# Kernel tuning notes

Hardware: AMD Instinct MI355X
Metric: run time of the kernel (lower is better)

The kernel has to match this reference:

```python
import math
import jax, jax.numpy as jnp
import numpy as np

N_GAUSS = 1_000_000
EPS = 1e-8


def setup_inputs() -> dict:
    key = jax.random.key(0)
    k1, k2, k3 = jax.random.split(key, 3)
    init_extent = 50.0
    means = (jax.random.uniform(k1, (N_GAUSS, 3), dtype=jnp.float32) - 0.5) * 2.0 * init_extent
    log_scales = jnp.full((N_GAUSS, 3), math.log(0.05), dtype=jnp.float32)
    quats = jax.random.normal(k2, (N_GAUSS, 4), dtype=jnp.float32)
    sh_coeffs = jax.random.normal(k3, (N_GAUSS, 16, 3), dtype=jnp.float32) * 0.01
    opa_logit = math.log(0.1 / 0.9)  # inverse_sigmoid(init_opacity=0.1)
    opacity_camera = jnp.full((N_GAUSS, 1), opa_logit, dtype=jnp.float32)
    opacity_lidar = jnp.full((N_GAUSS, 1), opa_logit, dtype=jnp.float32)
    camera_to_world = jnp.eye(4, dtype=jnp.float32)
    lidar_to_world = jnp.eye(4, dtype=jnp.float32)
    intrinsics = jnp.array([[1000.0, 0.0, 800.0], [0.0, 1000.0, 450.0], [0.0, 0.0, 1.0]], dtype=jnp.float32)
    return dict(means=means, log_scales=log_scales, quats=quats, sh_coeffs=sh_coeffs,
                opacity_camera=opacity_camera, opacity_lidar=opacity_lidar,
                camera_to_world=camera_to_world, intrinsics=intrinsics,
                lidar_to_world=lidar_to_world,
                rgb_width=1600, rgb_height=900, lidar_width=1024, lidar_height=128,
                fov_min_deg=-25, fov_max_deg=3, near_plane=1, far_plane=100)


def _bilinear_scatter(u, v, w, vals, H, W, wrap_u):
    """Scatter vals [N,C] with weights w [N] at continuous pixel coords (u,v)
    using bilinear splatting. Returns [H, W, C+1] (weighted vals, weight sum)."""
    u0 = jnp.floor(u)
    v0 = jnp.floor(v)
    fu = u - u0
    fv = v - v0
    u0i = u0.astype(jnp.int32)
    v0i = v0.astype(jnp.int32)
    acc = jnp.zeros((H * W, vals.shape[-1] + 1), dtype=vals.dtype)
    corners = ((0, 0, (1.0 - fu) * (1.0 - fv)), (1, 0, fu * (1.0 - fv)),
               (0, 1, (1.0 - fu) * fv), (1, 1, fu * fv))
    for du, dv, cw in corners:
        ui = u0i + du
        vi = v0i + dv
        if wrap_u:
            ui = jnp.mod(ui, W)
            ok_u = jnp.ones_like(ui, dtype=bool)
        else:
            ok_u = (ui >= 0) & (ui < W)
        ok = ok_u & (vi >= 0) & (vi < H)
        ww = w * cw * ok.astype(w.dtype)
        idx = jnp.clip(vi, 0, H - 1) * W + jnp.clip(ui, 0, W - 1)
        payload = jnp.concatenate([vals * ww[:, None], ww[:, None]], axis=-1)
        acc = acc.at[idx].add(payload)
    return acc.reshape(H, W, -1)


def reference(means, log_scales, quats, sh_coeffs, opacity_camera, opacity_lidar,
              camera_to_world, intrinsics, lidar_to_world,
              rgb_width, rgb_height, lidar_width, lidar_height,
              fov_min_deg, fov_max_deg, near_plane, far_plane):
    H, W = int(rgb_height), int(rgb_width)
    HL, WL = int(lidar_height), int(lidar_width)
    near = float(near_plane)
    far = float(far_plane)

    # ---- camera (point-splat proxy of gsplat rasterization) ----
    w2c = jnp.linalg.inv(camera_to_world)
    pts_c = means @ w2c[:3, :3].T + w2c[:3, 3]  # [N,3] camera frame
    x, y, z = pts_c[:, 0], pts_c[:, 1], pts_c[:, 2]
    valid_c = (z > near) & (z < far)
    zs = jnp.where(valid_c, z, 1.0)
    u = intrinsics[0, 0] * x / zs + intrinsics[0, 2]
    v = intrinsics[1, 1] * y / zs + intrinsics[1, 2]
    opa_c = jax.nn.sigmoid(jnp.clip(opacity_camera[:, 0], -20.0, 20.0))
    colors = jax.nn.sigmoid(sh_coeffs[:, 0, :])  # DC band, as in render_rgb
    wc = opa_c * valid_c.astype(opa_c.dtype)
    vals_c = jnp.concatenate([colors, z[:, None]], axis=-1)  # [N,4] (rgb, depth)
    acc = _bilinear_scatter(u, v, wc, vals_c, H, W, wrap_u=False)
    wsum = acc[..., 4]
    alpha = jnp.clip(wsum, 0.0, 1.0)
    rgb = acc[..., :3] / (wsum[..., None] + EPS) * alpha[..., None]  # black background
    depth = acc[..., 3] / (wsum + EPS)

    # ---- LiDAR (custom spherical bilinear range-image splat, mean aggregation) ----
    w2l = jnp.linalg.inv(lidar_to_world)
    pts_l = means @ w2l[:3, :3].T + w2l[:3, 3]
    r = jnp.linalg.norm(pts_l, axis=-1)
    az = jnp.arctan2(pts_l[:, 1], pts_l[:, 0])
    el = jnp.arcsin(pts_l[:, 2] / jnp.maximum(r, 1e-6))
    fmin = math.radians(float(fov_min_deg))
    fmax = math.radians(float(fov_max_deg))
    uL = (az / (2.0 * jnp.pi) + 0.5) * WL          # azimuth wraps around
    vL = (fmax - el) / (fmax - fmin) * (HL - 1)    # elevation row
    valid_l = (r > near) & (r < far) & (el >= fmin) & (el <= fmax)
    opa_l = jax.nn.sigmoid(jnp.clip(opacity_lidar[:, 0], -20.0, 20.0))
    wl = opa_l * valid_l.astype(opa_l.dtype)
    acc_l = _bilinear_scatter(uL, vL, wl, r[:, None], HL, WL, wrap_u=True)
    lw = acc_l[..., 1]
    lidar_depth = acc_l[..., 0] / (lw + EPS)  # 'mean' depth aggregation
    lidar_alpha = jnp.clip(lw, 0.0, 1.0)

    return (rgb, depth, alpha, lidar_depth, lidar_alpha)
```

## Files before the change

### kernel.cpp

```cpp
#include <hip/hip_runtime.h>
#include <math.h>

#define EPSV 1e-8f
#define PI_D 3.14159265358979323846

#define HW_C  (1600LL * 900LL)
#define LHW_C (1024LL * 128LL)

__device__ __forceinline__ void invert4x4_reg(const float* __restrict__ m,
                                              float* __restrict__ out) {
    double a00=m[0], a01=m[1], a02=m[2], a03=m[3];
    double a10=m[4], a11=m[5], a12=m[6], a13=m[7];
    double a20=m[8], a21=m[9], a22=m[10],a23=m[11];
    double a30=m[12],a31=m[13],a32=m[14],a33=m[15];

    double b00 = a00*a11 - a01*a10;
    double b01 = a00*a12 - a02*a10;
    double b02 = a00*a13 - a03*a10;
    double b03 = a01*a12 - a02*a11;
    double b04 = a01*a13 - a03*a11;
    double b05 = a02*a13 - a03*a12;
    double b06 = a20*a31 - a21*a30;
    double b07 = a20*a32 - a22*a30;
    double b08 = a20*a33 - a23*a30;
    double b09 = a21*a32 - a22*a31;
    double b10 = a21*a33 - a23*a31;
    double b11 = a22*a33 - a23*a32;

    double det = b00*b11 - b01*b10 + b02*b09 + b03*b08 - b04*b07 + b05*b06;
    double inv = 1.0 / det;

    out[0]  = (float)(( a11*b11 - a12*b10 + a13*b09) * inv);
    out[1]  = (float)((-a01*b11 + a02*b10 - a03*b09) * inv);
    out[2]  = (float)(( a31*b05 - a32*b04 + a33*b03) * inv);
    out[3]  = (float)((-a21*b05 + a22*b04 - a23*b03) * inv);
    out[4]  = (float)((-a10*b11 + a12*b08 - a13*b07) * inv);
    out[5]  = (float)(( a00*b11 - a02*b08 + a03*b07) * inv);
    out[6]  = (float)((-a30*b05 + a32*b02 - a33*b01) * inv);
    out[7]  = (float)(( a20*b05 - a22*b02 + a23*b01) * inv);
    out[8]  = (float)(( a10*b10 - a11*b08 + a13*b06) * inv);
    out[9]  = (float)((-a00*b10 + a01*b08 - a03*b06) * inv);
    out[10] = (float)(( a30*b04 - a31*b02 + a33*b00) * inv);
    out[11] = (float)((-a20*b04 + a21*b02 - a23*b00) * inv);
    out[12] = (float)((-a10*b09 + a11*b07 - a12*b06) * inv);
    out[13] = (float)(( a00*b09 - a01*b07 + a02*b06) * inv);
    out[14] = (float)((-a30*b03 + a31*b01 - a32*b00) * inv);
    out[15] = (float)(( a20*b03 - a21*b01 + a22*b00) * inv);
}

__global__ void prep_kernel(const float* __restrict__ c2w,
                            const float* __restrict__ l2w,
                            float* __restrict__ ws) {
    if (blockIdx.x == 0 && threadIdx.x == 0) {
        invert4x4_reg(c2w, ws);
        invert4x4_reg(l2w, ws + 16);
    }
}

__device__ __forceinline__ float sigmoid_clipped(float x) {
    #pragma clang fp contract(off)
    x = fminf(fmaxf(x, -20.0f), 20.0f);
    return 1.0f / (1.0f + expf(-x));
}

__global__ __launch_bounds__(256) void scatter_ws_kernel(
    const float* __restrict__ means,
    const float* __restrict__ sh,
    const float* __restrict__ opa_c,
    const float* __restrict__ opa_l,
    const float* __restrict__ intr,
    const float* __restrict__ ws,
    const int* __restrict__ p_W, const int* __restrict__ p_H,
    const int* __restrict__ p_WL, const int* __restrict__ p_HL,
    const int* __restrict__ p_fmin, const int* __restrict__ p_fmax,
    const int* __restrict__ p_near, const int* __restrict__ p_far,
    float* __restrict__ acc, int N)
{
    #pragma clang fp contract(off)
    const int i = blockIdx.x * blockDim.x + threadIdx.x;
    if (i >= N) return;

    const int W = *p_W, H = *p_H, WL = *p_WL, HL = *p_HL;
    const float nearp = (float)(*p_near);
    const float farp  = (float)(*p_far);
    const double dfmin = (double)(*p_fmin) * PI_D / 180.0;
    const double dfmax = (double)(*p_fmax) * PI_D / 180.0;
    const float ffmin  = (float)dfmin;
    const float ffmax  = (float)dfmax;
    const float denomL = (float)(dfmax - dfmin);
    const float twopi  = (float)(2.0 * PI_D);

    const long long HW = (long long)W * H;
    float* __restrict__ lacc = acc + 8 * HW;

    const float px = means[3 * i + 0];
    const float py = means[3 * i + 1];
    const float pz = means[3 * i + 2];
    const float* w2c = ws;
    const float* w2l = ws + 16;

    {
        float x = w2c[0] * px + w2c[1] * py + w2c[2]  * pz + w2c[3];
        float y = w2c[4] * px + w2c[5] * py + w2c[6]  * pz + w2c[7];
        float z = w2c[8] * px + w2c[9] * py + w2c[10] * pz + w2c[11];
        if (z > nearp && z < farp) {
            float u = intr[0] * x / z + intr[2];
            float v = intr[4] * y / z + intr[5];
            float wc = sigmoid_clipped(opa_c[i]);
            const float* shp = sh + 48LL * i;
            float c0 = 1.0f / (1.0f + expf(-shp[0]));
            float c1 = 1.0f / (1.0f + expf(-shp[1]));
            float c2 = 1.0f / (1.0f + expf(-shp[2]));

            float u0f = floorf(u), v0f = floorf(v);
            float fu = u - u0f, fv = v - v0f;
            int u0 = (int)u0f, v0 = (int)v0f;
            #pragma unroll
            for (int c = 0; c < 4; c++) {
                int du = c & 1, dv = c >> 1;
                int ui = u0 + du, vi = v0 + dv;
                if (ui >= 0 && ui < W && vi >= 0 && vi < H) {
                    float cw = (du ? fu : 1.0f - fu) * (dv ? fv : 1.0f - fv);
                    float ww = wc * cw;
                    float* rec = acc + 8LL * ((long long)vi * W + ui);
                    atomicAdd(rec + 0, c0 * ww);
                    atomicAdd(rec + 1, c1 * ww);
                    atomicAdd(rec + 2, c2 * ww);
                    atomicAdd(rec + 3, z * ww);
                    atomicAdd(rec + 4, ww);
                }
            }
        }
    }

    {
        float x = w2l[0] * px + w2l[1] * py + w2l[2]  * pz + w2l[3];
        float y = w2l[4] * px + w2l[5] * py + w2l[6]  * pz + w2l[7];
        float z = w2l[8] * px + w2l[9] * py + w2l[10] * pz + w2l[11];
        float rr = ((x * x) + (y * y)) + (z * z);
        float r = sqrtf(rr);
        float q  = z / fmaxf(r, 1e-6f);
        float el = (float)asin((double)q);
        if (r > nearp && r < farp && el >= ffmin && el <= ffmax) {
            float az = (float)atan2((double)y, (double)x);
            float uL = (az / twopi + 0.5f) * (float)WL;
            float vL = (ffmax - el) / denomL * (float)(HL - 1);
            float wl = sigmoid_clipped(opa_l[i]);

            float u0f = floorf(uL), v0f = floorf(vL);
            float fu = uL - u0f, fv = vL - v0f;
            int u0 = (int)u0f, v0 = (int)v0f;
            #pragma unroll
            for (int c = 0; c < 4; c++) {
                int du = c & 1, dv = c >> 1;
                int ui = u0 + du, vi = v0 + dv;
                ui %= WL; if (ui < 0) ui += WL;
                if (vi >= 0 && vi < HL) {
                    float cw = (du ? fu : 1.0f - fu) * (dv ? fv : 1.0f - fv);
                    float ww = wl * cw;
                    float* rec = lacc + 2LL * ((long long)vi * WL + ui);
                    atomicAdd(rec + 0, r * ww);
                    atomicAdd(rec + 1, ww);
                }
            }
        }
    }
}

__global__ __launch_bounds__(256) void finalize_ws_kernel(
    const float* __restrict__ acc,
    float* __restrict__ out,
    const int* __restrict__ p_W, const int* __restrict__ p_H,
    const int* __restrict__ p_WL, const int* __restrict__ p_HL)
{
    const int W = *p_W, H = *p_H, WL = *p_WL, HL = *p_HL;
    const long long HW = (long long)W * H;
    const long long LHW = (long long)WL * HL;
    const float* __restrict__ lacc = acc + 8 * HW;

    long long i = (long long)blockIdx.x * blockDim.x + threadIdx.x;
    if (i < HW) {
        const float* rec = acc + 8 * i;
        float r0 = rec[0], r1 = rec[1], r2 = rec[2], zw = rec[3], wsum = rec[4];
        float a = fminf(fmaxf(wsum, 0.0f), 1.0f);
        float inv = 1.0f / (wsum + EPSV);
        float s = inv * a;
        out[3 * i + 0] = r0 * s;
        out[3 * i + 1] = r1 * s;
        out[3 * i + 2] = r2 * s;
        out[3 * HW + i] = zw * inv;
        out[4 * HW + i] = a;
    }
    if (i < LHW) {
        float rw = lacc[2 * i], wsum = lacc[2 * i + 1];
        out[5 * HW + i]       = rw * (1.0f / (wsum + EPSV));
        out[5 * HW + LHW + i] = fminf(fmaxf(wsum, 0.0f), 1.0f);
    }
}

__global__ __launch_bounds__(256) void scatter_kernel(
    const float* __restrict__ means,
    const float* __restrict__ sh,
    const float* __restrict__ opa_c,
    const float* __restrict__ opa_l,
    const float* __restrict__ intr,
    const float* __restrict__ ws,
    const int* __restrict__ p_W, const int* __restrict__ p_H,
    const int* __restrict__ p_WL, const int* __restrict__ p_HL,
    const int* __restrict__ p_fmin, const int* __restrict__ p_fmax,
    const int* __restrict__ p_near, const int* __restrict__ p_far,
    float* __restrict__ out, int N)
{
    #pragma clang fp contract(off)
    const int i = blockIdx.x * blockDim.x + threadIdx.x;
    if (i >= N) return;

    const int W = *p_W, H = *p_H, WL = *p_WL, HL = *p_HL;
    const float nearp = (float)(*p_near);
    const float farp  = (float)(*p_far);
    const double dfmin = (double)(*p_fmin) * PI_D / 180.0;
    const double dfmax = (double)(*p_fmax) * PI_D / 180.0;
    const float ffmin  = (float)dfmin;
    const float ffmax  = (float)dfmax;
    const float denomL = (float)(dfmax - dfmin);
    const float twopi  = (float)(2.0 * PI_D);

    const long long HW = (long long)W * H;
    const long long LHW = (long long)WL * HL;
    const long long depthOff = 3 * HW;
    const long long alphaOff = 4 * HW;
    const long long ldOff    = 5 * HW;
    const long long laOff    = 5 * HW + LHW;

    const float px = means[3 * i + 0];
    const float py = means[3 * i + 1];
    const float pz = means[3 * i + 2];
    const float* w2c = ws;
    const float* w2l = ws + 16;

    {
        float x = w2c[0] * px + w2c[1] * py + w2c[2]  * pz + w2c[3];
        float y = w2c[4] * px + w2c[5] * py + w2c[6]  * pz + w2c[7];
        float z = w2c[8] * px + w2c[9] * py + w2c[10] * pz + w2c[11];
        if (z > nearp && z < farp) {
            float u = intr[0] * x / z + intr[2];
            float v = intr[4] * y / z + intr[5];
            float wc = sigmoid_clipped(opa_c[i]);
            const float* shp = sh + 48LL * i;
            float c0 = 1.0f / (1.0f + expf(-shp[0]));
            float c1 = 1.0f / (1.0f + expf(-shp[1]));
            float c2 = 1.0f / (1.0f + expf(-shp[2]));

            float u0f = floorf(u), v0f = floorf(v);
            float fu = u - u0f, fv = v - v0f;
            int u0 = (int)u0f, v0 = (int)v0f;
            #pragma unroll
            for (int c = 0; c < 4; c++) {
                int du = c & 1, dv = c >> 1;
                int ui = u0 + du, vi = v0 + dv;
                if (ui >= 0 && ui < W && vi >= 0 && vi < H) {
                    float cw = (du ? fu : 1.0f - fu) * (dv ? fv : 1.0f - fv);
                    float ww = wc * cw;
                    long long idx = (long long)vi * W + ui;
                    atomicAdd(&out[idx * 3 + 0], c0 * ww);
                    atomicAdd(&out[idx * 3 + 1], c1 * ww);
                    atomicAdd(&out[idx * 3 + 2], c2 * ww);
                    atomicAdd(&out[depthOff + idx], z * ww);
                    atomicAdd(&out[alphaOff + idx], ww);
                }
            }
        }
    }
    {
        float x = w2l[0] * px + w2l[1] * py + w2l[2]  * pz + w2l[3];
        float y = w2l[4] * px + w2l[5] * py + w2l[6]  * pz + w2l[7];
        float z = w2l[8] * px + w2l[9] * py + w2l[10] * pz + w2l[11];
        float rr = ((x * x) + (y * y)) + (z * z);
        float r = sqrtf(rr);
        float q  = z / fmaxf(r, 1e-6f);
        float el = (float)asin((double)q);
        if (r > nearp && r < farp && el >= ffmin && el <= ffmax) {
            float az = (float)atan2((double)y, (double)x);
            float uL = (az / twopi + 0.5f) * (float)WL;
            float vL = (ffmax - el) / denomL * (float)(HL - 1);
            float wl = sigmoid_clipped(opa_l[i]);

            float u0f = floorf(uL), v0f = floorf(vL);
            float fu = uL - u0f, fv = vL - v0f;
            int u0 = (int)u0f, v0 = (int)v0f;
            #pragma unroll
            for (int c = 0; c < 4; c++) {
                int du = c & 1, dv = c >> 1;
                int ui = u0 + du, vi = v0 + dv;
                ui %= WL; if (ui < 0) ui += WL;
                if (vi >= 0 && vi < HL) {
                    float cw = (du ? fu : 1.0f - fu) * (dv ? fv : 1.0f - fv);
                    float ww = wl * cw;
                    long long idx = (long long)vi * WL + ui;
                    atomicAdd(&out[ldOff + idx], r * ww);
                    atomicAdd(&out[laOff + idx], ww);
                }
            }
        }
    }
}

__global__ __launch_bounds__(256) void finalize_kernel(
    float* __restrict__ out,
    const int* __restrict__ p_W, const int* __restrict__ p_H,
    const int* __restrict__ p_WL, const int* __restrict__ p_HL)
{
    const int W = *p_W, H = *p_H, WL = *p_WL, HL = *p_HL;
    const long long HW = (long long)W * H;
    const long long LHW = (long long)WL * HL;

    long long i = (long long)blockIdx.x * blockDim.x + threadIdx.x;
    if (i < HW) {
        float wsum = out[4 * HW + i];
        float a = fminf(fmaxf(wsum, 0.0f), 1.0f);
        float inv = 1.0f / (wsum + EPSV);
        float s = inv * a;
        out[3 * i + 0] *= s;
        out[3 * i + 1] *= s;
        out[3 * i + 2] *= s;
        out[3 * HW + i] *= inv;
        out[4 * HW + i] = a;
    }
    if (i < LHW) {
        float wsum = out[5 * HW + LHW + i];
        out[5 * HW + i] *= 1.0f / (wsum + EPSV);
        out[5 * HW + LHW + i] = fminf(fmaxf(wsum, 0.0f), 1.0f);
    }
}

extern "C" void kernel_launch(void* const* d_in, const int* in_sizes, int n_in,
                              void* d_out, int out_size, void* d_ws, size_t ws_size,
                              hipStream_t stream) {
    const float* means  = (const float*)d_in[0];
    const float* sh     = (const float*)d_in[3];
    const float* opa_c  = (const float*)d_in[4];
    const float* opa_l  = (const float*)d_in[5];
    const float* c2w    = (const float*)d_in[6];
    const float* intr   = (const float*)d_in[7];
    const float* l2w    = (const float*)d_in[8];
    const int* p_W    = (const int*)d_in[9];
    const int* p_H    = (const int*)d_in[10];
    const int* p_WL   = (const int*)d_in[11];
    const int* p_HL   = (const int*)d_in[12];
    const int* p_fmin = (const int*)d_in[13];
    const int* p_fmax = (const int*)d_in[14];
    const int* p_near = (const int*)d_in[15];
    const int* p_far  = (const int*)d_in[16];

    const int N = in_sizes[0] / 3;
    float* out = (float*)d_out;
    float* ws  = (float*)d_ws;

    const size_t accFloats = 8 * (size_t)HW_C + 2 * (size_t)LHW_C;
    const size_t wsNeeded  = (32 + accFloats) * sizeof(float);
    const bool fast = (ws_size >= wsNeeded);

    prep_kernel<<<1, 64, 0, stream>>>(c2w, l2w, ws);

    if (fast) {
        float* acc = ws + 32;
        hipMemsetAsync(acc, 0, accFloats * sizeof(float), stream);
        scatter_ws_kernel<<<(N + 255) / 256, 256, 0, stream>>>(
            means, sh, opa_c, opa_l, intr, ws,
            p_W, p_H, p_WL, p_HL, p_fmin, p_fmax, p_near, p_far,
            acc, N);
        finalize_ws_kernel<<<(int)((HW_C + 255) / 256), 256, 0, stream>>>(
            acc, out, p_W, p_H, p_WL, p_HL);
    } else {
        hipMemsetAsync(d_out, 0, (size_t)out_size * sizeof(float), stream);
        scatter_kernel<<<(N + 255) / 256, 256, 0, stream>>>(
            means, sh, opa_c, opa_l, intr, ws,
            p_W, p_H, p_WL, p_HL, p_fmin, p_fmax, p_near, p_far,
            out, N);
        finalize_kernel<<<(int)((HW_C + 255) / 256), 256, 0, stream>>>(
            out, p_W, p_H, p_WL, p_HL);
    }
}
```

Before: 426.8 us.

## Replicate LiDAR accumulator per XCC and pack camera records to five floats

Camera accumulator records shrink from 8 to 5 floats per pixel, cutting memset and finalize traffic. The LiDAR range-image accumulator is replicated per XCC, selected via a hardware register read, and atomics use workgroup scope so they resolve in the local L2 instead of contending across dies. Finalize sums the eight replicas. Correctness depends on workgroup-scope atomics being coherent within an XCC's L2 and on a kernel boundary flushing those partial sums before finalize reads them.

```diff
diff --git a/kernel.cpp b/kernel.cpp
--- a/kernel.cpp
+++ b/kernel.cpp
@@ -6,6 +6,15 @@
 
 #define HW_C  (1600LL * 900LL)
 #define LHW_C (1024LL * 128LL)
+#define NREP  8
+
+__device__ __forceinline__ int xcc_id() {
+    return (int)(__builtin_amdgcn_s_getreg(63508) & 7u);
+}
+
+__device__ __forceinline__ void l2_atomic_add(float* addr, float v) {
+    __hip_atomic_fetch_add(addr, v, __ATOMIC_RELAXED, __HIP_MEMORY_SCOPE_WORKGROUP);
+}
 
 __device__ __forceinline__ void invert4x4_reg(const float* __restrict__ m,
                                               float* __restrict__ out) {
@@ -74,7 +83,7 @@
     const int* __restrict__ p_WL, const int* __restrict__ p_HL,
     const int* __restrict__ p_fmin, const int* __restrict__ p_fmax,
     const int* __restrict__ p_near, const int* __restrict__ p_far,
-    float* __restrict__ acc, int N)
+    float* __restrict__ cam, int N)
 {
     #pragma clang fp contract(off)
     const int i = blockIdx.x * blockDim.x + threadIdx.x;
@@ -90,8 +99,9 @@
     const float denomL = (float)(dfmax - dfmin);
     const float twopi  = (float)(2.0 * PI_D);
 
-    const long long HW = (long long)W * H;
-    float* __restrict__ lacc = acc + 8 * HW;
+    const long long HW  = (long long)W * H;
+    const long long LHW = (long long)WL * HL;
+    float* __restrict__ lrep = cam + 5 * HW + (long long)xcc_id() * (2 * LHW);
 
     const float px = means[3 * i + 0];
     const float py = means[3 * i + 1];
@@ -122,7 +132,7 @@
                 if (ui >= 0 && ui < W && vi >= 0 && vi < H) {
                     float cw = (du ? fu : 1.0f - fu) * (dv ? fv : 1.0f - fv);
                     float ww = wc * cw;
-                    float* rec = acc + 8LL * ((long long)vi * W + ui);
+                    float* rec = cam + 5LL * ((long long)vi * W + ui);
                     atomicAdd(rec + 0, c0 * ww);
                     atomicAdd(rec + 1, c1 * ww);
                     atomicAdd(rec + 2, c2 * ww);
@@ -158,9 +168,9 @@
                 if (vi >= 0 && vi < HL) {
                     float cw = (du ? fu : 1.0f - fu) * (dv ? fv : 1.0f - fv);
                     float ww = wl * cw;
-                    float* rec = lacc + 2LL * ((long long)vi * WL + ui);
-                    atomicAdd(rec + 0, r * ww);
-                    atomicAdd(rec + 1, ww);
+                    float* rec = lrep + 2LL * ((long long)vi * WL + ui);
+                    l2_atomic_add(rec + 0, r * ww);
+                    l2_atomic_add(rec + 1, ww);
                 }
             }
         }
@@ -168,19 +178,19 @@
 }
 
 __global__ __launch_bounds__(256) void finalize_ws_kernel(
-    const float* __restrict__ acc,
+    const float* __restrict__ cam,
     float* __restrict__ out,
     const int* __restrict__ p_W, const int* __restrict__ p_H,
     const int* __restrict__ p_WL, const int* __restrict__ p_HL)
 {
     const int W = *p_W, H = *p_H, WL = *p_WL, HL = *p_HL;
-    const long long HW = (long long)W * H;
+    const long long HW  = (long long)W * H;
     const long long LHW = (long long)WL * HL;
-    const float* __restrict__ lacc = acc + 8 * HW;
+    const float* __restrict__ lid = cam + 5 * HW;
 
     long long i = (long long)blockIdx.x * blockDim.x + threadIdx.x;
     if (i < HW) {
-        const float* rec = acc + 8 * i;
+        const float* rec = cam + 5 * i;
         float r0 = rec[0], r1 = rec[1], r2 = rec[2], zw = rec[3], wsum = rec[4];
         float a = fminf(fmaxf(wsum, 0.0f), 1.0f);
         float inv = 1.0f / (wsum + EPSV);
@@ -192,7 +202,13 @@
         out[4 * HW + i] = a;
     }
     if (i < LHW) {
-        float rw = lacc[2 * i], wsum = lacc[2 * i + 1];
+        float rw = 0.0f, wsum = 0.0f;
+        #pragma unroll
+        for (int k = 0; k < NREP; k++) {
+            const float* rep = lid + (long long)k * (2 * LHW);
+            rw   += rep[2 * i];
+            wsum += rep[2 * i + 1];
+        }
         out[5 * HW + i]       = rw * (1.0f / (wsum + EPSV));
         out[5 * HW + LHW + i] = fminf(fmaxf(wsum, 0.0f), 1.0f);
     }
@@ -356,21 +372,21 @@
     float* out = (float*)d_out;
     float* ws  = (float*)d_ws;
 
-    const size_t accFloats = 8 * (size_t)HW_C + 2 * (size_t)LHW_C;
+    const size_t accFloats = 5 * (size_t)HW_C + (size_t)NREP * 2 * (size_t)LHW_C;
     const size_t wsNeeded  = (32 + accFloats) * sizeof(float);
     const bool fast = (ws_size >= wsNeeded);
 
     prep_kernel<<<1, 64, 0, stream>>>(c2w, l2w, ws);
 
     if (fast) {
-        float* acc = ws + 32;
-        hipMemsetAsync(acc, 0, accFloats * sizeof(float), stream);
+        float* cam = ws + 32;
+        hipMemsetAsync(cam, 0, accFloats * sizeof(float), stream);
         scatter_ws_kernel<<<(N + 255) / 256, 256, 0, stream>>>(
             means, sh, opa_c, opa_l, intr, ws,
             p_W, p_H, p_WL, p_HL, p_fmin, p_fmax, p_near, p_far,
-            acc, N);
+            cam, N);
         finalize_ws_kernel<<<(int)((HW_C + 255) / 256), 256, 0, stream>>>(
-            acc, out, p_W, p_H, p_WL, p_HL);
+            cam, out, p_W, p_H, p_WL, p_HL);
     } else {
         hipMemsetAsync(d_out, 0, (size_t)out_size * sizeof(float), stream);
         scatter_kernel<<<(N + 255) / 256, 256, 0, stream>>>(
```

Result: no change. 425.0 us (-0.4%).
